# Performance work log

Hardware: AMD Instinct MI355X
Metric: run time of the kernel (lower is better)

The kernel has to match this reference:

```python
import jax, jax.numpy as jnp
import numpy as np


def _shift(x, k):
    # roll time axis forward by k, zero-filling the first k steps
    if k == 0:
        return x
    return jnp.pad(x, ((0, 0), (k, 0), (0, 0)))[:, : x.shape[1]]


def _stu_conv(u, v, n):
    # u: (B,L,D), v: (L,K) spectral filters; non-tensordot branch of conv()
    B, L, D = u.shape
    K = v.shape[1]
    sgn = jnp.where(jnp.arange(L) % 2 == 1, -1.0, 1.0).astype(jnp.float32)[None, :, None, None]
    ue = jnp.broadcast_to(u[:, :, None, :], (B, L, K, D)).astype(jnp.float32)
    U = jnp.stack([ue, ue * sgn], axis=-1)                     # (B,L,K,D,2)
    Uf = jnp.fft.rfft(U, n=n, axis=1)
    vf = jnp.fft.rfft(v.astype(jnp.float32)[None, :, :, None, None], n=n, axis=1)
    Uc = jnp.fft.irfft(vf * Uf, n=n, axis=1)[:, :L]            # (B,L,K,D,2)
    U_plus = Uc[..., 0]
    U_minus = Uc[..., 1] * sgn
    return U_plus.astype(u.dtype), U_minus.astype(u.dtype)


def setup_inputs() -> dict:
    key = jax.random.key(0)
    ks = jax.random.split(key, 6)
    B, L, D, K, k_u, k_y = 2, 1024, 512, 16, 3, 2
    u = jax.random.normal(ks[0], (B, L, D), jnp.float32)
    filters = jax.random.normal(ks[1], (L, K), jnp.float32) / np.float32(np.sqrt(L))
    M_u = jax.random.normal(ks[2], (D, k_u, D), jnp.float32) * 0.01
    M_y = jax.random.normal(ks[3], (D, k_y, D), jnp.float32) * 0.01
    M_phi_plus = jax.random.normal(ks[4], (K, D, D), jnp.float32) * 0.01
    M_phi_minus = jax.random.normal(ks[5], (K, D, D), jnp.float32) * 0.01
    return {"u": u, "filters": filters, "M_u": M_u, "M_y": M_y,
            "M_phi_plus": M_phi_plus, "M_phi_minus": M_phi_minus}


def reference(u, filters, M_u, M_y, M_phi_plus, M_phi_minus):
    B, L, D = u.shape
    n = 1 << int(np.ceil(np.log2(2 * L - 1)))  # nearest power of two >= 2L-1
    k_u = M_u.shape[1]
    k_y = M_y.shape[1]

    # FFT-based long convolution with the +/- sign trick
    U_plus, U_minus = _stu_conv(u, filters, n)
    spectral = (jnp.einsum('blkd,kdo->blo', U_plus, M_phi_plus)
                + jnp.einsum('blkd,kdo->blo', U_minus, M_phi_minus))

    # input-AR term of compute_ar_strict: sum_j u[t+1-j] @ M_u[:, j-1].T (shifts 0..k_u-1)
    u_sh = jnp.stack([_shift(u, j - 1) for j in range(1, k_u + 1)], axis=1)  # (B,k_u,L,D)
    y_in = jnp.einsum('bjlf,ijf->bli', u_sh, M_u)

    z = spectral + y_in  # (B,L,D)

    # output-AR recurrence of compute_ar_strict as a scan
    def step(y_buf, z_t):
        y_t = z_t + jnp.einsum('bjf,djf->bd', y_buf, M_y)
        y_buf = jnp.concatenate([y_t[:, None], y_buf[:, :-1]], axis=1)
        return y_buf, y_t

    _, ys = jax.lax.scan(step, jnp.zeros((B, k_y, D), z.dtype), jnp.swapaxes(z, 0, 1))
    return jnp.swapaxes(ys, 0, 1)  # (B,L,D)
```

## Files before the change

kernel.cpp:

```cpp
#include <hip/hip_runtime.h>
#include <hip/hip_bf16.h>


using bf16 = __hip_bfloat16;
typedef __attribute__((ext_vector_type(8))) short bf16x8;
typedef __attribute__((ext_vector_type(4))) float f32x4;

#define B_   2
#define L_   1024
#define D_   512
#define K_   16
#define KT   17920
#define ROWS 2048
#define NTAP 6
#define PBLD 3584
#define ZTLD 3072
#define SPLITD 16
#define SPLITR 8

#define WAIT_VM4 0x0F74
#define WAIT_VM0 0x0F70

__device__ __forceinline__ void gll16(const void* g, void* l) {
    __builtin_amdgcn_global_load_lds(
        (const __attribute__((address_space(1))) unsigned int*)g,
        (__attribute__((address_space(3))) unsigned int*)l, 16, 0, 0);
}

__global__ void prep_ew(const float* __restrict__ u, const float* __restrict__ fil,
                        const float* __restrict__ Mu, const float* __restrict__ My,
                        bf16* __restrict__ U, bf16* __restrict__ BT,
                        bf16* __restrict__ PB, bf16* __restrict__ W,
                        bf16* __restrict__ Myb) {
    int bid = blockIdx.x, tid = threadIdx.x;
    auto pack4 = [](float4 v) {
        ushort4 o; bf16 h;
        h = __float2bfloat16(v.x); o.x = *(unsigned short*)&h;
        h = __float2bfloat16(v.y); o.y = *(unsigned short*)&h;
        h = __float2bfloat16(v.z); o.z = *(unsigned short*)&h;
        h = __float2bfloat16(v.w); o.w = *(unsigned short*)&h;
        return o;
    };
    if (bid < 3072) {
        int e4 = bid * 256 + tid;
        int r = e4 / 384, rem = e4 % 384;
        int t = rem >> 7, f = (rem & 127) * 4;
        int b = r >> 10, l = r & 1023;
        float4 v = {0.f, 0.f, 0.f, 0.f};
        if (l >= t) v = *(const float4*)&u[((size_t)b * L_ + l - t) * D_ + f];
        *(ushort4*)&U[(size_t)r * KT + 16384 + t * 512 + f] = pack4(v);
    } else if (bid < 3840) {
        int e4 = (bid - 3072) * 256 + tid;
        int o = e4 / 384, tf4 = (e4 % 384) * 4;
        float4 v = *(const float4*)&Mu[(size_t)o * 1536 + tf4];
        *(ushort4*)&BT[(size_t)o * KT + 16384 + tf4] = pack4(v);
    } else if (bid < 4352) {
        int e4 = (bid - 3840) * 256 + tid;
        int n = e4 >> 8, c4 = (e4 & 255) * 4;
        float4 v;
        if (c4 < 512) {
            v.x = (n == c4) ? 1.f : 0.f;     v.y = (n == c4 + 1) ? 1.f : 0.f;
            v.z = (n == c4 + 2) ? 1.f : 0.f; v.w = (n == c4 + 3) ? 1.f : 0.f;
        } else v = *(const float4*)&My[(size_t)n * 1024 + (c4 - 512)];
        *(ushort4*)&PB[(size_t)n * PBLD + c4] = pack4(v);
    } else if (bid < 5120) {
        int tile = bid - 4352;
        int set = tile >> 8, rem = tile & 255;
        int k = rem >> 4, g = (rem >> 2) & 3, kb = rem & 3;
        for (int idx = tid; idx < 4096; idx += 256) {
            int i = idx >> 5, jp = idx & 31;
            int j = ((jp >> 3) ^ ((i >> 1) & 3)) * 8 + (jp & 7);
            int x = g * 128 + i - kb * 32 - j - (set == 2 ? 1 : 0);
            float v = 0.f;
            if (x >= 0) {
                int row = (set == 0) ? 2 * x : 2 * x + 1;
                v = fil[row * K_ + k];
            }
            W[(size_t)tile * 4096 + idx] = __float2bfloat16(v);
        }
    } else {
        int e4 = (bid - 5120) * 256 + tid;
        float4 v = *(const float4*)&My[(size_t)e4 * 4];
        *(ushort4*)&Myb[(size_t)e4 * 4] = pack4(v);
    }
}

__global__ void prep_tr(const float* __restrict__ Mp, const float* __restrict__ Mm,
                        const float* __restrict__ My, const float* __restrict__ u,
                        bf16* __restrict__ BT, bf16* __restrict__ BTT,
                        bf16* __restrict__ uPT) {
    __shared__ bf16 t[64][72];
    int zb = blockIdx.z;
    int col = threadIdx.x & 63, r0 = (threadIdx.x >> 6) * 16;
    if (zb < 32) {
        int dt = blockIdx.x * 64, ot = blockIdx.y * 64, c = zb;
        int k = c & 15;
        const float* sp = Mp + (size_t)k * D_ * D_;
        const float* sm = Mm + (size_t)k * D_ * D_;
        float sg = (c < 16) ? 1.f : -1.f;
        for (int i = 0; i < 16; ++i) {
            size_t o_ = (size_t)(dt + r0 + i) * D_ + ot + col;
            t[r0 + i][col] = __float2bfloat16(sp[o_] + sg * sm[o_]);
        }
        __syncthreads();
        for (int i = 0; i < 16; ++i)
            BT[(size_t)(ot + r0 + i) * KT + c * D_ + dt + col] = t[col][r0 + i];
    } else if (zb < 34) {
        int h = zb - 32;
        int dt = blockIdx.x * 64, ft = blockIdx.y * 64;
        for (int i = 0; i < 16; ++i)
            t[r0 + i][col] = __float2bfloat16(My[(size_t)(dt + r0 + i) * 1024 + (1 - h) * 512 + ft + col]);
        __syncthreads();
        for (int i = 0; i < 16; ++i)
            BTT[(size_t)(ft + r0 + i) * 1024 + h * 512 + dt + col] = t[col][r0 + i];
    } else {
        for (int it = 0; it < 4; ++it) {
            int b = it >> 1, p = it & 1;
            int mt = blockIdx.x * 64, dt = blockIdx.y * 64;
            __syncthreads();
            for (int i = 0; i < 16; ++i)
                t[r0 + i][col] = __float2bfloat16(u[((size_t)b * L_ + 2 * (mt + r0 + i) + p) * D_ + dt + col]);
            __syncthreads();
            for (int i = 0; i < 16; ++i)
                uPT[((size_t)it * 512 + dt + r0 + i) * 512 + mt + col] = t[col][r0 + i];
        }
    }
}

__device__ __forceinline__ void phi_body(
    const bf16* A, int lda, const bf16* BT, int ldb,
    bf16* out, int ldo, int klen, const bf16* add, int lad,
    int row0, int col0, bf16* sA, bf16* sB)
{
    const int tid = threadIdx.x, lane = tid & 63, wave = tid >> 6;
    const int wm = (wave & 1) * 64, wn = (wave >> 1) * 64;
    const int ml = lane & 15, q = lane >> 4;
    const int srow = lane >> 2, scol = (((lane & 3) ^ ((srow >> 1) & 3))) * 8;
    const int swz = ((ml >> 1) & 3);
    f32x4 acc[4][4] = {};

    for (int k = 0; k < klen; k += 32) {
        __syncthreads();
        #pragma unroll
        for (int repi = 0; repi < 2; ++repi) {
            int a = wave + repi * 4;
            gll16(A  + (size_t)(row0 + a * 16 + srow) * lda + k + scol, &sA[a * 512]);
            gll16(BT + (size_t)(col0 + a * 16 + srow) * ldb + k + scol, &sB[a * 512]);
        }
        __syncthreads();
        bf16x8 af[4], bfr[4];
        #pragma unroll
        for (int i = 0; i < 4; ++i)
            af[i] = *(const bf16x8*)&sA[(wm + i * 16 + ml) * 32 + (q ^ swz) * 8];
        #pragma unroll
        for (int j = 0; j < 4; ++j)
            bfr[j] = *(const bf16x8*)&sB[(wn + j * 16 + ml) * 32 + (q ^ swz) * 8];
        #pragma unroll
        for (int i = 0; i < 4; ++i)
            #pragma unroll
            for (int j = 0; j < 4; ++j)
                acc[i][j] = __builtin_amdgcn_mfma_f32_16x16x32_bf16(af[i], bfr[j], acc[i][j], 0, 0, 0);
    }
    #pragma unroll
    for (int i = 0; i < 4; ++i)
        #pragma unroll
        for (int j = 0; j < 4; ++j)
            #pragma unroll
            for (int reg = 0; reg < 4; ++reg) {
                int r = row0 + wm + i * 16 + q * 4 + reg;
                int cc = col0 + wn + j * 16 + ml;
                float v = acc[i][j][reg];
                if (add) v += __bfloat162float(add[(size_t)r * lad + cc]);
                out[(size_t)r * ldo + cc] = __float2bfloat16(v);
            }
}

__global__ void k_ztaps(const bf16* __restrict__ partD, float* __restrict__ z,
                        bf16* __restrict__ ZT, bf16* PB, const bf16* BTT) {
    __shared__ bf16 sA[4096];
    __shared__ bf16 sB[4096];
    int bid = blockIdx.x;
    if (bid < 32) {
        int row0 = (bid & 3) * 128, col0 = (bid >> 2) * 128;
        phi_body(PB + 3 * 512, PBLD, BTT, 1024, PB + 5 * 512, PBLD, 1024,
                 nullptr, 0, row0, col0, sA, sB);
        return;
    }
    int t = (bid - 32) * 256 + threadIdx.x;
    int r = t >> 7, f4 = (t & 127) * 4;
    const ushort4* p = (const ushort4*)partD;
    float4 s = {0.f, 0.f, 0.f, 0.f};
    #pragma unroll
    for (int c = 0; c < SPLITD; ++c) {
        ushort4 v = p[(size_t)c * (ROWS * D_ / 4) + t];
        s.x += __uint_as_float((unsigned)v.x << 16);
        s.y += __uint_as_float((unsigned)v.y << 16);
        s.z += __uint_as_float((unsigned)v.z << 16);
        s.w += __uint_as_float((unsigned)v.w << 16);
    }
    ((float4*)z)[t] = s;
    ushort4 zb;
    { bf16 h;
      h = __float2bfloat16(s.x); zb.x = *(unsigned short*)&h;
      h = __float2bfloat16(s.y); zb.y = *(unsigned short*)&h;
      h = __float2bfloat16(s.z); zb.z = *(unsigned short*)&h;
      h = __float2bfloat16(s.w); zb.w = *(unsigned short*)&h; }
    int l = r & 1023;
    #pragma unroll
    for (int sh = 1; sh <= NTAP; ++sh)
        if (l + sh < 1024)
            *(ushort4*)&ZT[(size_t)(r + sh) * ZTLD + (sh - 1) * 512 + f4] = zb;
    ushort4 z4 = {0, 0, 0, 0};
    for (int sh = l + 1; sh <= NTAP; ++sh)
        *(ushort4*)&ZT[(size_t)r * ZTLD + (sh - 1) * 512 + f4] = z4;
}

__global__ void reduce_out(const float* __restrict__ z, const bf16* __restrict__ partR,
                           float* __restrict__ out) {
    int t = blockIdx.x * 256 + threadIdx.x;
    if (t >= ROWS * D_ / 4) return;
    float4 s = ((const float4*)z)[t];
    const ushort4* p = (const ushort4*)partR;
    #pragma unroll
    for (int c = 0; c < SPLITR; ++c) {
        ushort4 v = p[(size_t)c * (ROWS * D_ / 4) + t];
        s.x += __uint_as_float((unsigned)v.x << 16);
        s.y += __uint_as_float((unsigned)v.y << 16);
        s.z += __uint_as_float((unsigned)v.z << 16);
        s.w += __uint_as_float((unsigned)v.w << 16);
    }
    ((float4*)out)[t] = s;
}

__global__ __launch_bounds__(256, 3) void conv_misc(
    const bf16* __restrict__ W, const bf16* __restrict__ uPT,
    bf16* __restrict__ U,
    const bf16* PB, const bf16* BTT, const bf16* Myb)
{
    __shared__ bf16 sA[3][4096];
    __shared__ bf16 sB[3][4096];
    const int z = blockIdx.z;
    if (z < 3) {
        int row0 = blockIdx.x * 128, col0 = blockIdx.y * 128;
        bf16* BTTw = (bf16*)BTT; bf16* PBw = (bf16*)PB;
        if (z == 0)
            phi_body(PB, PBLD, BTT, 1024, PBw + 2 * 512, PBLD, 1024,
                     nullptr, 0, row0, col0, &sA[0][0], &sB[0][0]);
        else if (z == 1)
            phi_body(BTT + 512, 1024, Myb + 512, 1024,
                     BTTw + (size_t)512 * 1024, 1024, 512,
                     nullptr, 0, row0, col0, &sA[0][0], &sB[0][0]);
        else
            phi_body(BTT + 512, 1024, Myb, 1024,
                     BTTw + (size_t)512 * 1024 + 512, 1024, 512,
                     BTT, 1024, row0, col0, &sA[0][0], &sB[0][0]);
        return;
    }
    const int zc = z - 3;
    const int mt = 3 - blockIdx.x, dt = blockIdx.y * 128;
    const int t = zc & 3, b = (zc >> 2) & 1, k = zc >> 3;
    const int pb_ = t & 1;
    const int p = (t & 1) ^ (t >> 1);
    const int set = (t < 2) ? 0 : (t == 2 ? 1 : 2);
    const int ch = (t < 2) ? k : 16 + k;
    const int plane = b * 2 + pb_;
    const int tid = threadIdx.x, lane = tid & 63, wave = tid >> 6;
    const int wm = (wave & 1) * 64, wn = (wave >> 1) * 64;
    const int ml = lane & 15, q = lane >> 4;
    const int srow = lane >> 2, scol = (((lane & 3) ^ ((srow >> 1) & 3))) * 8;
    const int swz = ((ml >> 1) & 3);
    f32x4 acc[4][4] = {};
    const int n = (mt + 1) * 4;

    const bf16* bB0 = uPT + ((size_t)plane * 512 + dt + wave * 16       + srow) * 512 + scol;
    const bf16* bB1 = uPT + ((size_t)plane * 512 + dt + (wave + 4) * 16 + srow) * 512 + scol;
    const bf16* wbase = W + ((size_t)(set * 16 + k) * 16) * 4096;
    auto stage = [&](int s, int buf) {
        const bf16* wt = wbase + ((size_t)((mt - (s >> 2)) * 4 + (s & 3))) * 4096;
        gll16(wt + wave * 512 + lane * 8, &sA[buf][wave * 512]);
        gll16(wt + (wave + 4) * 512 + lane * 8, &sA[buf][(wave + 4) * 512]);
        gll16(bB0 + s * 32, &sB[buf][wave * 512]);
        gll16(bB1 + s * 32, &sB[buf][(wave + 4) * 512]);
    };
    auto compute = [&](int c) {
        bf16x8 af[4], bfr[4];
        #pragma unroll
        for (int i = 0; i < 4; ++i)
            af[i] = *(const bf16x8*)&sA[c][(wm + i * 16 + ml) * 32 + (q ^ swz) * 8];
        #pragma unroll
        for (int j = 0; j < 4; ++j)
            bfr[j] = *(const bf16x8*)&sB[c][(wn + j * 16 + ml) * 32 + (q ^ swz) * 8];
        #pragma unroll
        for (int i = 0; i < 4; ++i)
            #pragma unroll
            for (int j = 0; j < 4; ++j)
                acc[i][j] = __builtin_amdgcn_mfma_f32_16x16x32_bf16(af[i], bfr[j], acc[i][j], 0, 0, 0);
    };
    stage(0, 0); stage(1, 1);
    int c = 0, nb = 2;
    for (int i = 0; i < n - 1; ++i) {
        __builtin_amdgcn_s_waitcnt(WAIT_VM4);
        __builtin_amdgcn_s_barrier();
        if (i + 2 < n) stage(i + 2, nb);
        compute(c);
        c = (c == 2) ? 0 : c + 1; nb = (nb == 2) ? 0 : nb + 1;
    }
    __builtin_amdgcn_s_waitcnt(WAIT_VM0);
    __builtin_amdgcn_s_barrier();
    compute(c);

    #pragma unroll
    for (int i = 0; i < 4; ++i)
        #pragma unroll
        for (int j = 0; j < 4; ++j)
            #pragma unroll
            for (int reg = 0; reg < 4; ++reg) {
                int m = mt * 128 + wm + i * 16 + q * 4 + reg;
                int l = 2 * m + p;
                int d = dt + wn + j * 16 + ml;
                U[(size_t)(b * L_ + l) * KT + ch * 512 + d] = __float2bfloat16(acc[i][j][reg]);
            }
}

__global__ __launch_bounds__(256, 3) void gemm_k(
    const bf16* __restrict__ A, int lda,
    const bf16* __restrict__ BT, int ldb,
    bf16* __restrict__ part, int k_chunk, int zoff,
    const bf16* PB, const bf16* BTT)
{
    __shared__ bf16 sA[3][4096];
    __shared__ bf16 sB[3][4096];
    if (zoff && blockIdx.z == 0) {
        int x = blockIdx.x;
        if (x >= 8) return;
        int row0 = (x & 3) * 128;
        int col0 = (((x >> 2) * 4) + blockIdx.y) * 128;
        phi_body(PB + 512, PBLD, BTT, 1024, (bf16*)PB + 3 * 512, PBLD, 1024,
                 nullptr, 0, row0, col0, &sA[0][0], &sB[0][0]);
        return;
    }
    const int zz = blockIdx.z - zoff;
    const int row0 = blockIdx.x * 128, col0 = blockIdx.y * 128;
    const int k0 = zz * k_chunk;
    const int n = k_chunk >> 5;
    const int tid = threadIdx.x, lane = tid & 63, wave = tid >> 6;
    const int wm = (wave & 1) * 64, wn = (wave >> 1) * 64;
    const int ml = lane & 15, q = lane >> 4;
    const int srow = lane >> 2, scol = (((lane & 3) ^ ((srow >> 1) & 3))) * 8;
    const int swz = ((ml >> 1) & 3);
    f32x4 acc[4][4] = {};

    const bf16* bA0 = A  + (size_t)(row0 + wave * 16       + srow) * lda + k0 + scol;
    const bf16* bA1 = A  + (size_t)(row0 + (wave + 4) * 16 + srow) * lda + k0 + scol;
    const bf16* bB0 = BT + (size_t)(col0 + wave * 16       + srow) * ldb + k0 + scol;
    const bf16* bB1 = BT + (size_t)(col0 + (wave + 4) * 16 + srow) * ldb + k0 + scol;
    auto stage = [&](int s, int buf) {
        gll16(bA0 + s * 32, &sA[buf][wave * 512]);
        gll16(bA1 + s * 32, &sA[buf][(wave + 4) * 512]);
        gll16(bB0 + s * 32, &sB[buf][wave * 512]);
        gll16(bB1 + s * 32, &sB[buf][(wave + 4) * 512]);
    };
    auto compute = [&](int c) {
        bf16x8 af[4], bfr[4];
        #pragma unroll
        for (int i = 0; i < 4; ++i)
            af[i] = *(const bf16x8*)&sA[c][(wm + i * 16 + ml) * 32 + (q ^ swz) * 8];
        #pragma unroll
        for (int j = 0; j < 4; ++j)
            bfr[j] = *(const bf16x8*)&sB[c][(wn + j * 16 + ml) * 32 + (q ^ swz) * 8];
        #pragma unroll
        for (int i = 0; i < 4; ++i)
            #pragma unroll
            for (int j = 0; j < 4; ++j)
                acc[i][j] = __builtin_amdgcn_mfma_f32_16x16x32_bf16(af[i], bfr[j], acc[i][j], 0, 0, 0);
    };
    stage(0, 0); stage(1, 1);
    int c = 0, nb = 2;
    for (int i = 0; i < n - 1; ++i) {
        __builtin_amdgcn_s_waitcnt(WAIT_VM4);
        __builtin_amdgcn_s_barrier();
        if (i + 2 < n) stage(i + 2, nb);
        compute(c);
        c = (c == 2) ? 0 : c + 1; nb = (nb == 2) ? 0 : nb + 1;
    }
    __builtin_amdgcn_s_waitcnt(WAIT_VM0);
    __builtin_amdgcn_s_barrier();
    compute(c);

    bf16* o = part + (size_t)zz * ROWS * D_;
    #pragma unroll
    for (int i = 0; i < 4; ++i)
        #pragma unroll
        for (int j = 0; j < 4; ++j)
            #pragma unroll
            for (int reg = 0; reg < 4; ++reg) {
                int r = row0 + wm + i * 16 + q * 4 + reg;
                int cc = col0 + wn + j * 16 + ml;
                o[(size_t)r * D_ + cc] = __float2bfloat16(acc[i][j][reg]);
            }
}

extern "C" void kernel_launch(void* const* d_in, const int* in_sizes, int n_in,
                              void* d_out, int out_size, void* d_ws, size_t ws_size,
                              hipStream_t stream) {
    const float* u   = (const float*)d_in[0];
    const float* fil = (const float*)d_in[1];
    const float* Mu  = (const float*)d_in[2];
    const float* My  = (const float*)d_in[3];
    const float* Mp  = (const float*)d_in[4];
    const float* Mm  = (const float*)d_in[5];
    float* out = (float*)d_out;

    char* ws = (char*)d_ws;
    size_t off = 0;
    auto alloc = [&](size_t bytes) { void* p = ws + off; off = (off + bytes + 255) & ~(size_t)255; return p; };
    bf16*  U    = (bf16*) alloc((size_t)ROWS * KT * 2);
    bf16*  BT   = (bf16*) alloc((size_t)512 * KT * 2);
    bf16*  PB   = (bf16*) alloc((size_t)512 * PBLD * 2);
    bf16*  BTT  = (bf16*) alloc((size_t)1024 * 1024 * 2);
    bf16*  Myb  = (bf16*) alloc((size_t)512 * 1024 * 2);
    float* z    = (float*)alloc((size_t)ROWS * D_ * 4);
    bf16*  ZT   = (bf16*) alloc((size_t)ROWS * ZTLD * 2);
    char*  region = (char*)alloc((size_t)SPLITD * ROWS * D_ * 2);
    bf16*  W    = (bf16*)region;
    bf16*  uPT  = (bf16*)(region + (size_t)768 * 4096 * 2);
    bf16*  partD = (bf16*)region;
    bf16*  partR = (bf16*)region;

    prep_ew<<<5632, 256, 0, stream>>>(u, fil, Mu, My, U, BT, PB, W, Myb);
    prep_tr<<<dim3(8, 8, 35), 256, 0, stream>>>(Mp, Mm, My, u, BT, BTT, uPT);

    conv_misc<<<dim3(4, 4, 131), 256, 0, stream>>>(W, uPT, U, PB, BTT, Myb);

    gemm_k<<<dim3(16, 4, SPLITD + 1), 256, 0, stream>>>(U, KT, BT, KT, partD,
                                                        KT / SPLITD, 1, PB, BTT);

    k_ztaps<<<1056, 256, 0, stream>>>(partD, z, ZT, PB, BTT);

    gemm_k<<<dim3(16, 4, SPLITR), 256, 0, stream>>>(ZT, ZTLD, PB + 512, PBLD,
                                                    partR, ZTLD / SPLITR, 0,
                                                    nullptr, nullptr);

    reduce_out<<<(ROWS * D_ / 4 + 255) / 256, 256, 0, stream>>>(z, partR, out);
}
```

Measured before the change: 259.5 us.

## Widen GEMM tiles to 128x256 and replace materialized tap matrix with shifted z buffer

The conv and split-K GEMM kernels now use 128x256 output tiles, with each wave computing a 64x128 block and loading four B rows per stage, so A-tile loads are reused across twice as many columns. Launch bounds drop to 2 blocks per SM because of the larger accumulators and LDS. The replicated ZT tap matrix, which wrote each z row six times, is replaced by a single zero-padded bf16 z buffer. The AR GEMM reads it through row-shifted base pointers, and SPLITR becomes 12 with each chunk covering one tap and half of K. This removes redundant z writes, but lower occupancy and fewer blocks per launch could reduce latency hiding.

```diff
diff --git a/kernel.cpp b/kernel.cpp
--- a/kernel.cpp
+++ b/kernel.cpp
@@ -14,11 +14,11 @@
 #define ROWS 2048
 #define NTAP 6
 #define PBLD 3584
-#define ZTLD 3072
 #define SPLITD 16
-#define SPLITR 8
-
-#define WAIT_VM4 0x0F74
+#define SPLITR 12
+#define ZBROWS 1032
+
+#define WAIT_VM6 0x0F76
 #define WAIT_VM0 0x0F70
 
 __device__ __forceinline__ void gll16(const void* g, void* l) {
@@ -176,7 +176,7 @@
 }
 
 __global__ void k_ztaps(const bf16* __restrict__ partD, float* __restrict__ z,
-                        bf16* __restrict__ ZT, bf16* PB, const bf16* BTT) {
+                        bf16* __restrict__ zbuf, bf16* PB, const bf16* BTT) {
     __shared__ bf16 sA[4096];
     __shared__ bf16 sB[4096];
     int bid = blockIdx.x;
@@ -186,7 +186,17 @@
                  nullptr, 0, row0, col0, sA, sB);
         return;
     }
-    int t = (bid - 32) * 256 + threadIdx.x;
+    if (bid == 32) {
+        ushort4 z4 = {0, 0, 0, 0};
+        for (int i = 0; i < 8; ++i) {
+            int e4 = i * 256 + threadIdx.x;
+            int b = e4 >> 10, rem = e4 & 1023;
+            int g = rem >> 7, c4 = (rem & 127) * 4;
+            *(ushort4*)&zbuf[(size_t)(b * ZBROWS + g) * 512 + c4] = z4;
+        }
+        return;
+    }
+    int t = (bid - 33) * 256 + threadIdx.x;
     int r = t >> 7, f4 = (t & 127) * 4;
     const ushort4* p = (const ushort4*)partD;
     float4 s = {0.f, 0.f, 0.f, 0.f};
@@ -199,20 +209,14 @@
         s.w += __uint_as_float((unsigned)v.w << 16);
     }
     ((float4*)z)[t] = s;
-    ushort4 zb;
+    ushort4 zb4;
     { bf16 h;
-      h = __float2bfloat16(s.x); zb.x = *(unsigned short*)&h;
-      h = __float2bfloat16(s.y); zb.y = *(unsigned short*)&h;
-      h = __float2bfloat16(s.z); zb.z = *(unsigned short*)&h;
-      h = __float2bfloat16(s.w); zb.w = *(unsigned short*)&h; }
-    int l = r & 1023;
-    #pragma unroll
-    for (int sh = 1; sh <= NTAP; ++sh)
-        if (l + sh < 1024)
-            *(ushort4*)&ZT[(size_t)(r + sh) * ZTLD + (sh - 1) * 512 + f4] = zb;
-    ushort4 z4 = {0, 0, 0, 0};
-    for (int sh = l + 1; sh <= NTAP; ++sh)
-        *(ushort4*)&ZT[(size_t)r * ZTLD + (sh - 1) * 512 + f4] = z4;
+      h = __float2bfloat16(s.x); zb4.x = *(unsigned short*)&h;
+      h = __float2bfloat16(s.y); zb4.y = *(unsigned short*)&h;
+      h = __float2bfloat16(s.z); zb4.z = *(unsigned short*)&h;
+      h = __float2bfloat16(s.w); zb4.w = *(unsigned short*)&h; }
+    int b = r >> 10, li = r & 1023;
+    *(ushort4*)&zbuf[(size_t)(b * ZBROWS + 8 + li) * 512 + f4] = zb4;
 }
 
 __global__ void reduce_out(const float* __restrict__ z, const bf16* __restrict__ partR,
@@ -232,21 +236,23 @@
     ((float4*)out)[t] = s;
 }
 
-__global__ __launch_bounds__(256, 3) void conv_misc(
+__global__ __launch_bounds__(256, 2) void conv_misc(
     const bf16* __restrict__ W, const bf16* __restrict__ uPT,
     bf16* __restrict__ U,
     const bf16* PB, const bf16* BTT, const bf16* Myb)
 {
     __shared__ bf16 sA[3][4096];
-    __shared__ bf16 sB[3][4096];
+    __shared__ bf16 sB[3][8192];
     const int z = blockIdx.z;
-    if (z < 3) {
-        int row0 = blockIdx.x * 128, col0 = blockIdx.y * 128;
+    if (z < 6) {
+        int which = z >> 1;
+        int row0 = blockIdx.x * 128;
+        int col0 = ((z & 1) * 2 + blockIdx.y) * 128;
         bf16* BTTw = (bf16*)BTT; bf16* PBw = (bf16*)PB;
-        if (z == 0)
+        if (which == 0)
             phi_body(PB, PBLD, BTT, 1024, PBw + 2 * 512, PBLD, 1024,
                      nullptr, 0, row0, col0, &sA[0][0], &sB[0][0]);
-        else if (z == 1)
+        else if (which == 1)
             phi_body(BTT + 512, 1024, Myb + 512, 1024,
                      BTTw + (size_t)512 * 1024, 1024, 512,
                      nullptr, 0, row0, col0, &sA[0][0], &sB[0][0]);
@@ -256,8 +262,8 @@
                      BTT, 1024, row0, col0, &sA[0][0], &sB[0][0]);
         return;
     }
-    const int zc = z - 3;
-    const int mt = 3 - blockIdx.x, dt = blockIdx.y * 128;
+    const int zc = z - 6;
+    const int mt = 3 - blockIdx.x, dt2 = blockIdx.y;
     const int t = zc & 3, b = (zc >> 2) & 1, k = zc >> 3;
     const int pb_ = t & 1;
     const int p = (t & 1) ^ (t >> 1);
@@ -265,41 +271,44 @@
     const int ch = (t < 2) ? k : 16 + k;
     const int plane = b * 2 + pb_;
     const int tid = threadIdx.x, lane = tid & 63, wave = tid >> 6;
-    const int wm = (wave & 1) * 64, wn = (wave >> 1) * 64;
+    const int wm = (wave & 1) * 64, wn = (wave >> 1) * 128;
     const int ml = lane & 15, q = lane >> 4;
     const int srow = lane >> 2, scol = (((lane & 3) ^ ((srow >> 1) & 3))) * 8;
     const int swz = ((ml >> 1) & 3);
-    f32x4 acc[4][4] = {};
+    f32x4 acc[4][8] = {};
     const int n = (mt + 1) * 4;
 
-    const bf16* bB0 = uPT + ((size_t)plane * 512 + dt + wave * 16       + srow) * 512 + scol;
-    const bf16* bB1 = uPT + ((size_t)plane * 512 + dt + (wave + 4) * 16 + srow) * 512 + scol;
+    const bf16* bB[4];
+    #pragma unroll
+    for (int r = 0; r < 4; ++r)
+        bB[r] = uPT + ((size_t)plane * 512 + dt2 * 256 + (wave + r * 4) * 16 + srow) * 512 + scol;
     const bf16* wbase = W + ((size_t)(set * 16 + k) * 16) * 4096;
     auto stage = [&](int s, int buf) {
         const bf16* wt = wbase + ((size_t)((mt - (s >> 2)) * 4 + (s & 3))) * 4096;
         gll16(wt + wave * 512 + lane * 8, &sA[buf][wave * 512]);
         gll16(wt + (wave + 4) * 512 + lane * 8, &sA[buf][(wave + 4) * 512]);
-        gll16(bB0 + s * 32, &sB[buf][wave * 512]);
-        gll16(bB1 + s * 32, &sB[buf][(wave + 4) * 512]);
+        #pragma unroll
+        for (int r = 0; r < 4; ++r)
+            gll16(bB[r] + s * 32, &sB[buf][(wave + r * 4) * 512]);
     };
     auto compute = [&](int c) {
-        bf16x8 af[4], bfr[4];
+        bf16x8 af[4], bfr[8];
         #pragma unroll
         for (int i = 0; i < 4; ++i)
             af[i] = *(const bf16x8*)&sA[c][(wm + i * 16 + ml) * 32 + (q ^ swz) * 8];
         #pragma unroll
-        for (int j = 0; j < 4; ++j)
+        for (int j = 0; j < 8; ++j)
             bfr[j] = *(const bf16x8*)&sB[c][(wn + j * 16 + ml) * 32 + (q ^ swz) * 8];
         #pragma unroll
         for (int i = 0; i < 4; ++i)
             #pragma unroll
-            for (int j = 0; j < 4; ++j)
+            for (int j = 0; j < 8; ++j)
                 acc[i][j] = __builtin_amdgcn_mfma_f32_16x16x32_bf16(af[i], bfr[j], acc[i][j], 0, 0, 0);
     };
     stage(0, 0); stage(1, 1);
     int c = 0, nb = 2;
     for (int i = 0; i < n - 1; ++i) {
-        __builtin_amdgcn_s_waitcnt(WAIT_VM4);
+        __builtin_amdgcn_s_waitcnt(WAIT_VM6);
         __builtin_amdgcn_s_barrier();
         if (i + 2 < n) stage(i + 2, nb);
         compute(c);
@@ -312,72 +321,84 @@
     #pragma unroll
     for (int i = 0; i < 4; ++i)
         #pragma unroll
-        for (int j = 0; j < 4; ++j)
+        for (int j = 0; j < 8; ++j)
             #pragma unroll
             for (int reg = 0; reg < 4; ++reg) {
                 int m = mt * 128 + wm + i * 16 + q * 4 + reg;
                 int l = 2 * m + p;
-                int d = dt + wn + j * 16 + ml;
+                int d = dt2 * 256 + wn + j * 16 + ml;
                 U[(size_t)(b * L_ + l) * KT + ch * 512 + d] = __float2bfloat16(acc[i][j][reg]);
             }
 }
 
-__global__ __launch_bounds__(256, 3) void gemm_k(
-    const bf16* __restrict__ A, int lda,
+__global__ __launch_bounds__(256, 2) void gemm_k(
+    const bf16* __restrict__ A, int lda, int k_chunk,
     const bf16* __restrict__ BT, int ldb,
-    bf16* __restrict__ part, int k_chunk, int zoff,
-    const bf16* PB, const bf16* BTT)
+    bf16* __restrict__ part,
+    const bf16* __restrict__ zbuf,
+    int zoff, const bf16* PB, const bf16* BTT)
 {
     __shared__ bf16 sA[3][4096];
-    __shared__ bf16 sB[3][4096];
+    __shared__ bf16 sB[3][8192];
     if (zoff && blockIdx.z == 0) {
         int x = blockIdx.x;
-        if (x >= 8) return;
         int row0 = (x & 3) * 128;
-        int col0 = (((x >> 2) * 4) + blockIdx.y) * 128;
+        int col0 = ((x >> 2) * 2 + blockIdx.y) * 128;
         phi_body(PB + 512, PBLD, BTT, 1024, (bf16*)PB + 3 * 512, PBLD, 1024,
                  nullptr, 0, row0, col0, &sA[0][0], &sB[0][0]);
         return;
     }
     const int zz = blockIdx.z - zoff;
-    const int row0 = blockIdx.x * 128, col0 = blockIdx.y * 128;
-    const int k0 = zz * k_chunk;
-    const int n = k_chunk >> 5;
+    const int row0 = blockIdx.x * 128, col0 = blockIdx.y * 256;
     const int tid = threadIdx.x, lane = tid & 63, wave = tid >> 6;
-    const int wm = (wave & 1) * 64, wn = (wave >> 1) * 64;
+    const int wm = (wave & 1) * 64, wn = (wave >> 1) * 128;
     const int ml = lane & 15, q = lane >> 4;
     const int srow = lane >> 2, scol = (((lane & 3) ^ ((srow >> 1) & 3))) * 8;
     const int swz = ((ml >> 1) & 3);
-    f32x4 acc[4][4] = {};
-
-    const bf16* bA0 = A  + (size_t)(row0 + wave * 16       + srow) * lda + k0 + scol;
-    const bf16* bA1 = A  + (size_t)(row0 + (wave + 4) * 16 + srow) * lda + k0 + scol;
-    const bf16* bB0 = BT + (size_t)(col0 + wave * 16       + srow) * ldb + k0 + scol;
-    const bf16* bB1 = BT + (size_t)(col0 + (wave + 4) * 16 + srow) * ldb + k0 + scol;
+    f32x4 acc[4][8] = {};
+
+    const bf16* Abase; int alda, n, k0;
+    if (zbuf) {
+        int s = 1 + (zz >> 1), koff = (zz & 1) * 256;
+        int b = row0 >> 10, li0 = row0 & 1023;
+        Abase = zbuf + ((size_t)(b * ZBROWS + 8 + li0 - s)) * 512 + koff;
+        alda = 512; n = 8; k0 = zz * 256;
+    } else {
+        Abase = A + (size_t)row0 * lda + (size_t)zz * k_chunk;
+        alda = lda; n = k_chunk >> 5; k0 = zz * k_chunk;
+    }
+    const bf16* bA0 = Abase + (size_t)(wave * 16 + srow) * alda + scol;
+    const bf16* bA1 = Abase + (size_t)((wave + 4) * 16 + srow) * alda + scol;
+    const bf16* bB[4];
+    #pragma unroll
+    for (int r = 0; r < 4; ++r)
+        bB[r] = BT + (size_t)(col0 + (wave + r * 4) * 16 + srow) * ldb + k0 + scol;
+
     auto stage = [&](int s, int buf) {
         gll16(bA0 + s * 32, &sA[buf][wave * 512]);
         gll16(bA1 + s * 32, &sA[buf][(wave + 4) * 512]);
-        gll16(bB0 + s * 32, &sB[buf][wave * 512]);
-        gll16(bB1 + s * 32, &sB[buf][(wave + 4) * 512]);
+        #pragma unroll
+        for (int r = 0; r < 4; ++r)
+            gll16(bB[r] + s * 32, &sB[buf][(wave + r * 4) * 512]);
     };
     auto compute = [&](int c) {
-        bf16x8 af[4], bfr[4];
+        bf16x8 af[4], bfr[8];
         #pragma unroll
         for (int i = 0; i < 4; ++i)
             af[i] = *(const bf16x8*)&sA[c][(wm + i * 16 + ml) * 32 + (q ^ swz) * 8];
         #pragma unroll
-        for (int j = 0; j < 4; ++j)
+        for (int j = 0; j < 8; ++j)
             bfr[j] = *(const bf16x8*)&sB[c][(wn + j * 16 + ml) * 32 + (q ^ swz) * 8];
         #pragma unroll
         for (int i = 0; i < 4; ++i)
             #pragma unroll
-            for (int j = 0; j < 4; ++j)
+            for (int j = 0; j < 8; ++j)
                 acc[i][j] = __builtin_amdgcn_mfma_f32_16x16x32_bf16(af[i], bfr[j], acc[i][j], 0, 0, 0);
     };
     stage(0, 0); stage(1, 1);
     int c = 0, nb = 2;
     for (int i = 0; i < n - 1; ++i) {
-        __builtin_amdgcn_s_waitcnt(WAIT_VM4);
+        __builtin_amdgcn_s_waitcnt(WAIT_VM6);
         __builtin_amdgcn_s_barrier();
         if (i + 2 < n) stage(i + 2, nb);
         compute(c);
@@ -391,7 +412,7 @@
     #pragma unroll
     for (int i = 0; i < 4; ++i)
         #pragma unroll
-        for (int j = 0; j < 4; ++j)
+        for (int j = 0; j < 8; ++j)
             #pragma unroll
             for (int reg = 0; reg < 4; ++reg) {
                 int r = row0 + wm + i * 16 + q * 4 + reg;
@@ -420,7 +441,7 @@
     bf16*  BTT  = (bf16*) alloc((size_t)1024 * 1024 * 2);
     bf16*  Myb  = (bf16*) alloc((size_t)512 * 1024 * 2);
     float* z    = (float*)alloc((size_t)ROWS * D_ * 4);
-    bf16*  ZT   = (bf16*) alloc((size_t)ROWS * ZTLD * 2);
+    bf16*  zb   = (bf16*) alloc((size_t)B_ * ZBROWS * 512 * 2);
     char*  region = (char*)alloc((size_t)SPLITD * ROWS * D_ * 2);
     bf16*  W    = (bf16*)region;
     bf16*  uPT  = (bf16*)(region + (size_t)768 * 4096 * 2);
@@ -430,16 +451,17 @@
     prep_ew<<<5632, 256, 0, stream>>>(u, fil, Mu, My, U, BT, PB, W, Myb);
     prep_tr<<<dim3(8, 8, 35), 256, 0, stream>>>(Mp, Mm, My, u, BT, BTT, uPT);
 
-    conv_misc<<<dim3(4, 4, 131), 256, 0, stream>>>(W, uPT, U, PB, BTT, Myb);
-
-    gemm_k<<<dim3(16, 4, SPLITD + 1), 256, 0, stream>>>(U, KT, BT, KT, partD,
-                                                        KT / SPLITD, 1, PB, BTT);
-
-    k_ztaps<<<1056, 256, 0, stream>>>(partD, z, ZT, PB, BTT);
-
-    gemm_k<<<dim3(16, 4, SPLITR), 256, 0, stream>>>(ZT, ZTLD, PB + 512, PBLD,
-                                                    partR, ZTLD / SPLITR, 0,
-                                                    nullptr, nullptr);
+    conv_misc<<<dim3(4, 2, 134), 256, 0, stream>>>(W, uPT, U, PB, BTT, Myb);
+
+    gemm_k<<<dim3(16, 2, SPLITD + 1), 256, 0, stream>>>(U, KT, KT / SPLITD,
+                                                        BT, KT, partD,
+                                                        nullptr, 1, PB, BTT);
+
+    k_ztaps<<<1057, 256, 0, stream>>>(partD, z, zb, PB, BTT);
+
+    gemm_k<<<dim3(16, 2, SPLITR), 256, 0, stream>>>(nullptr, 0, 256,
+                                                    PB + 512, PBLD, partR,
+                                                    zb, 0, nullptr, nullptr);
 
     reduce_out<<<(ROWS * D_ / 4 + 255) / 256, 256, 0, stream>>>(z, partR, out);
 }
```

New measurement: 273.5 us. +5.4%, slower.
